# Performance work log

Measured on AMD Instinct MI355X. Metric: run time of the kernel, lower is better.

## Reference

```python
import jax, jax.numpy as jnp
import numpy as np

NUM_LAYERS = 2
MAG = 5 / 10.0  # magnitude=5 on a 0-10 scale
FILL = 0.5      # gray fill for out-of-bounds pixels (images in [0,1])
ENH = 1.0 + 0.9 * MAG  # enhancement factor magnitude (brightness/contrast/sharpness)


def _bilinear(img, xi, yi):
    H, W, _ = img.shape
    x0 = jnp.floor(xi); y0 = jnp.floor(yi)
    wx = xi - x0; wy = yi - y0
    def gather(yy, xx):
        valid = (xx >= 0) & (xx <= W - 1) & (yy >= 0) & (yy <= H - 1)
        v = img[jnp.clip(yy, 0, H - 1).astype(jnp.int32),
                jnp.clip(xx, 0, W - 1).astype(jnp.int32)]
        return jnp.where(valid[..., None], v, FILL)
    return (gather(y0, x0) * ((1 - wx) * (1 - wy))[..., None]
            + gather(y0, x0 + 1) * (wx * (1 - wy))[..., None]
            + gather(y0 + 1, x0) * ((1 - wx) * wy)[..., None]
            + gather(y0 + 1, x0 + 1) * (wx * wy)[..., None])


def _affine(img, a, b, tx, c, d, ty):
    # inverse affine map about image center, bilinear resample
    H, W, _ = img.shape
    ys, xs = jnp.meshgrid(jnp.arange(H, dtype=jnp.float32),
                          jnp.arange(W, dtype=jnp.float32), indexing='ij')
    cx = (W - 1) * 0.5; cy = (H - 1) * 0.5
    xi = a * (xs - cx) + b * (ys - cy) + tx + cx
    yi = c * (xs - cx) + d * (ys - cy) + ty + cy
    return _bilinear(img, xi, yi)


def _blend(a, b, f):
    return jnp.clip(a + f * (b - a), 0.0, 1.0)


def _smooth(img):
    # 3x3 smoothing kernel used by PIL/TF sharpness
    k = jnp.array([[1., 1., 1.], [1., 5., 1.], [1., 1., 1.]], jnp.float32) / 13.0
    H, W, _ = img.shape
    p = jnp.pad(img, ((1, 1), (1, 1), (0, 0)), mode='edge')
    out = jnp.zeros_like(img)
    for i in range(3):
        for j in range(3):
            out = out + k[i, j] * p[i:i + H, j:j + W]
    return out


def _rotate(img, s):
    th = s * (30.0 * MAG) * (np.pi / 180.0)
    co, si = jnp.cos(th), jnp.sin(th)
    return _affine(img, co, si, 0.0, -si, co, 0.0)

def _shear_x(img, s):
    sh = s * 0.3 * MAG
    return _affine(img, 1.0, -sh, 0.0, 0.0, 1.0, 0.0)

def _shear_y(img, s):
    sh = s * 0.3 * MAG
    return _affine(img, 1.0, 0.0, 0.0, -sh, 1.0, 0.0)

def _trans_x(img, s):
    t = s * 0.3 * MAG * img.shape[1]
    return _affine(img, 1.0, 0.0, -t, 0.0, 1.0, 0.0)

def _trans_y(img, s):
    t = s * 0.3 * MAG * img.shape[0]
    return _affine(img, 1.0, 0.0, 0.0, 0.0, 1.0, -t)

def _brightness(img, s):
    f = jnp.where(s > 0, ENH, 1.0 / ENH)
    return _blend(jnp.zeros_like(img), img, f)

def _contrast(img, s):
    f = jnp.where(s > 0, ENH, 1.0 / ENH)
    return _blend(jnp.mean(img) * jnp.ones_like(img), img, f)

def _sharpness(img, s):
    f = jnp.where(s > 0, ENH, 1.0 / ENH)
    return _blend(_smooth(img), img, f)


BRANCHES = [_rotate, _shear_x, _shear_y, _trans_x, _trans_y,
            _brightness, _contrast, _sharpness]


def _apply_one(img, ops, signs):
    # img: [H,W,3]; ops, signs: [NUM_LAYERS]
    for l in range(NUM_LAYERS):
        s = (2 * signs[l] - 1).astype(jnp.float32)
        img = jax.lax.switch(ops[l], BRANCHES, img, s)
    return img


def setup_inputs() -> dict:
    key = jax.random.key(0)
    k1, k2, k3 = jax.random.split(key, 3)
    B, H, W = 64, 512, 512
    images = jax.random.uniform(k1, (B, H, W, 3), dtype=jnp.float32)
    op_ids = jax.random.randint(k2, (B, NUM_LAYERS), 0, len(BRANCHES), dtype=jnp.int32)
    signs = jax.random.randint(k3, (B, NUM_LAYERS), 0, 2, dtype=jnp.int32)
    return {"images": images, "op_ids": op_ids, "signs": signs}


def reference(images, op_ids, signs):
    return jax.vmap(_apply_one)(images, op_ids, signs)
```

## Files before the change

### kernel.cpp

```cpp
#include <hip/hip_runtime.h>
#include <math.h>

#define IMH 512
#define IMW 512
#define NIMG 64
#define NPIX (IMH*IMW)
#define NELEM (NPIX*3)
#define CXF 255.5f
#define CYF 255.5f
#define ENHF 1.45f
#define INVENHF (1.0f/1.45f)
#define FILLF 0.5f
#define MBPI0 64
#define TW 32
#define TH 32
#define MAXLDS 1800

struct F3 { float x, y, z; };

__device__ __forceinline__ F3 mk3(float v){ F3 r; r.x=v; r.y=v; r.z=v; return r; }

__device__ __forceinline__ F3 ldpix(const float* __restrict__ im, int y, int x){
  const float* p = im + (y*IMW + x)*3;
  F3 r; r.x=p[0]; r.y=p[1]; r.z=p[2]; return r;
}

__device__ __forceinline__ F3 clip01(F3 v){
  F3 r;
  r.x = fminf(fmaxf(v.x, 0.f), 1.f);
  r.y = fminf(fmaxf(v.y, 0.f), 1.f);
  r.z = fminf(fmaxf(v.z, 0.f), 1.f);
  return r;
}

__device__ __forceinline__ void affine_params(int op, float s,
    float& a, float& b, float& tx, float& c, float& d, float& ty){
  a = 1.f; b = 0.f; tx = 0.f; c = 0.f; d = 1.f; ty = 0.f;
  if (op == 0){
    a = 0.96592582628907f; b = s * 0.25881904510252f; c = -b; d = a;
  } else if (op == 1){
    b = -s * 0.15f;
  } else if (op == 2){
    c = -s * 0.15f;
  } else if (op == 3){
    tx = -s * 76.8f;
  } else if (op == 4){
    ty = -s * 76.8f;
  }
}

__device__ __forceinline__ F3 bilin_img(const float* __restrict__ im, float xi, float yi){
  float x0f = floorf(xi), y0f = floorf(yi);
  float wx = xi - x0f, wy = yi - y0f;
  float w00 = (1.f-wx)*(1.f-wy), w01 = wx*(1.f-wy);
  float w10 = (1.f-wx)*wy,       w11 = wx*wy;
  int x0 = (int)x0f, y0 = (int)y0f;
  F3 r;
  if (x0 >= 0 && y0 >= 0 && x0 < IMW-1 && y0 < IMH-1){
    const float* p0 = im + (y0*IMW + x0)*3;
    const float* p1 = p0 + IMW*3;
    r.x = w00*p0[0] + w01*p0[3] + w10*p1[0] + w11*p1[3];
    r.y = w00*p0[1] + w01*p0[4] + w10*p1[1] + w11*p1[4];
    r.z = w00*p0[2] + w01*p0[5] + w10*p1[2] + w11*p1[5];
  } else {
    r = mk3(0.f);
    #pragma unroll
    for (int cidx = 0; cidx < 4; cidx++){
      int dx = cidx & 1, dy = cidx >> 1;
      int xx = x0 + dx, yy = y0 + dy;
      float w = (dx ? wx : (1.f - wx)) * (dy ? wy : (1.f - wy));
      F3 v;
      if (xx >= 0 && xx < IMW && yy >= 0 && yy < IMH)
        v = ldpix(im, yy, xx);
      else
        v = mk3(FILLF);
      r.x += w * v.x; r.y += w * v.y; r.z += w * v.z;
    }
  }
  return r;
}

__device__ F3 eval0(const float* __restrict__ im, int op, float s, float mean0, int x, int y){
  if (op < 5){
    float a,b,tx,c,d,ty; affine_params(op, s, a, b, tx, c, d, ty);
    float fx = (float)x - CXF, fy = (float)y - CYF;
    return bilin_img(im, a*fx + b*fy + tx + CXF, c*fx + d*fy + ty + CYF);
  }
  F3 v = ldpix(im, y, x);
  float f = (s > 0.f) ? ENHF : INVENHF;
  if (op == 5){
    F3 r; r.x = f*v.x; r.y = f*v.y; r.z = f*v.z; return clip01(r);
  }
  if (op == 6){
    F3 r;
    r.x = mean0 + f*(v.x - mean0);
    r.y = mean0 + f*(v.y - mean0);
    r.z = mean0 + f*(v.z - mean0);
    return clip01(r);
  }
  F3 sm; sm.x = (5.f/13.f)*v.x; sm.y = (5.f/13.f)*v.y; sm.z = (5.f/13.f)*v.z;
  #pragma unroll
  for (int dy = -1; dy <= 1; dy++){
    #pragma unroll
    for (int dx = -1; dx <= 1; dx++){
      if (dx == 0 && dy == 0) continue;
      int yy = min(max(y + dy, 0), IMH-1);
      int xx = min(max(x + dx, 0), IMW-1);
      F3 q = ldpix(im, yy, xx);
      sm.x += (1.f/13.f)*q.x; sm.y += (1.f/13.f)*q.y; sm.z += (1.f/13.f)*q.z;
    }
  }
  F3 r;
  r.x = sm.x + f*(v.x - sm.x);
  r.y = sm.y + f*(v.y - sm.y);
  r.z = sm.z + f*(v.z - sm.z);
  return clip01(r);
}

__device__ __forceinline__ float block_reduce(float v){
  #pragma unroll
  for (int off = 32; off > 0; off >>= 1) v += __shfl_down(v, off, 64);
  __shared__ float sm[4];
  int lane = threadIdx.x & 63, wid = threadIdx.x >> 6;
  if (lane == 0) sm[wid] = v;
  __syncthreads();
  float r = 0.f;
  if (threadIdx.x == 0) r = sm[0] + sm[1] + sm[2] + sm[3];
  return r;
}

__global__ __launch_bounds__(256) void mean0_kernel(const float* __restrict__ images,
    const int* __restrict__ ops, float* __restrict__ means){
  int img = blockIdx.x / MBPI0;
  if (ops[2*img] != 6) return;
  const float4* im = (const float4*)(images + (size_t)img * NELEM);
  float s = 0.f;
  for (int i = (blockIdx.x % MBPI0)*256 + threadIdx.x; i < NELEM/4; i += MBPI0*256){
    float4 v = im[i];
    s += v.x + v.y + v.z + v.w;
  }
  s = block_reduce(s);
  if (threadIdx.x == 0) atomicAdd(&means[2*img], s * (1.0f/(float)NELEM));
}

__device__ __forceinline__ void store4(float* __restrict__ out, int img, int y, int xbase,
                                       const F3* res){
  float4 o0 = make_float4(res[0].x, res[0].y, res[0].z, res[1].x);
  float4 o1 = make_float4(res[1].y, res[1].z, res[2].x, res[2].y);
  float4 o2 = make_float4(res[2].z, res[3].x, res[3].y, res[3].z);
  float4* op = (float4*)(out + ((size_t)img * NPIX + (size_t)y * IMW + xbase) * 3);
  op[0] = o0; op[1] = o1; op[2] = o2;
}

__global__ __launch_bounds__(256) void apply_kernel(const float* __restrict__ images,
    const int* __restrict__ ops, const int* __restrict__ signs,
    float* __restrict__ means, float* __restrict__ out){
  int img  = blockIdx.x >> 8;
  int tile = blockIdx.x & 255;
  int tx0 = (tile & 15) * TW;
  int ty0 = (tile >> 4) * TH;
  const float* im = images + (size_t)img * NELEM;
  int op0 = ops[2*img], op1 = ops[2*img + 1];
  float s0 = signs[2*img]     ? 1.f : -1.f;
  float s1 = signs[2*img + 1] ? 1.f : -1.f;
  float mean0 = means[2*img];

  int row   = threadIdx.x >> 3;
  int xbase = tx0 + ((threadIdx.x & 7) << 2);
  int y     = ty0 + row;
  float f1 = (s1 > 0.f) ? ENHF : INVENHF;

  if (op1 == 5 || op1 == 6){
    F3 res[4];
    float ssum = 0.f;
    #pragma unroll
    for (int q = 0; q < 4; q++){
      F3 v = eval0(im, op0, s0, mean0, xbase + q, y);
      if (op1 == 5){
        F3 o; o.x = f1*v.x; o.y = f1*v.y; o.z = f1*v.z;
        res[q] = clip01(o);
      } else {
        res[q] = v;
        ssum += v.x + v.y + v.z;
      }
    }
    store4(out, img, y, xbase, res);
    if (op1 == 6){
      ssum = block_reduce(ssum);
      if (threadIdx.x == 0) atomicAdd(&means[2*img + 1], ssum * (1.0f/(float)NELEM));
    }
    return;
  }

  float a1=1.f,b1=0.f,txx=0.f,c1=0.f,d1=1.f,tyy=0.f;
  int bx0, by0, bx1, by1;
  if (op1 < 5){
    affine_params(op1, s1, a1, b1, txx, c1, d1, tyy);
    float xmin = 1e30f, xmax = -1e30f, ymin = 1e30f, ymax = -1e30f;
    #pragma unroll
    for (int i = 0; i < 4; i++){
      float fx = (float)(tx0 + (i & 1) * (TW - 1)) - CXF;
      float fy = (float)(ty0 + (i >> 1) * (TH - 1)) - CYF;
      float xi = a1*fx + b1*fy + txx + CXF;
      float yi = c1*fx + d1*fy + tyy + CYF;
      xmin = fminf(xmin, xi); xmax = fmaxf(xmax, xi);
      ymin = fminf(ymin, yi); ymax = fmaxf(ymax, yi);
    }
    bx0 = (int)floorf(xmin) - 1; bx1 = (int)floorf(xmax) + 2;
    by0 = (int)floorf(ymin) - 1; by1 = (int)floorf(ymax) + 2;
  } else {
    bx0 = tx0 - 1; bx1 = tx0 + TW; by0 = ty0 - 1; by1 = ty0 + TH;
  }
  bx0 = max(bx0, 0); by0 = max(by0, 0);
  bx1 = min(bx1, IMW - 1); by1 = min(by1, IMH - 1);
  int bw = bx1 - bx0 + 1, bh = by1 - by0 + 1;
  int nstage = (bw > 0 && bh > 0) ? bw * bh : 0;

  __shared__ float lds[MAXLDS * 3];
  for (int idx = threadIdx.x; idx < nstage; idx += 256){
    int iy = idx / bw;
    int ix = idx - iy * bw;
    F3 v = eval0(im, op0, s0, mean0, bx0 + ix, by0 + iy);
    lds[idx*3 + 0] = v.x; lds[idx*3 + 1] = v.y; lds[idx*3 + 2] = v.z;
  }
  __syncthreads();

  F3 res[4];
  #pragma unroll
  for (int q = 0; q < 4; q++){
    int x = xbase + q;
    F3 o;
    if (op1 < 5){
      float fx = (float)x - CXF, fy = (float)y - CYF;
      float xi = a1*fx + b1*fy + txx + CXF;
      float yi = c1*fx + d1*fy + tyy + CYF;
      float xf0 = floorf(xi), yf0 = floorf(yi);
      float wx = xi - xf0, wy = yi - yf0;
      float w00 = (1.f-wx)*(1.f-wy), w01 = wx*(1.f-wy);
      float w10 = (1.f-wx)*wy,       w11 = wx*wy;
      int x0 = (int)xf0, y0 = (int)yf0;
      if (x0 >= 0 && y0 >= 0 && x0 < IMW-1 && y0 < IMH-1){
        const float* q0 = lds + ((y0 - by0) * bw + (x0 - bx0)) * 3;
        const float* q1 = q0 + bw * 3;
        o.x = w00*q0[0] + w01*q0[3] + w10*q1[0] + w11*q1[3];
        o.y = w00*q0[1] + w01*q0[4] + w10*q1[1] + w11*q1[4];
        o.z = w00*q0[2] + w01*q0[5] + w10*q1[2] + w11*q1[5];
      } else {
        o = mk3(0.f);
        #pragma unroll
        for (int ci = 0; ci < 4; ci++){
          int dx = ci & 1, dy = ci >> 1;
          int xx = x0 + dx, yy = y0 + dy;
          float w = (dx ? wx : (1.f - wx)) * (dy ? wy : (1.f - wy));
          F3 v;
          if (xx >= 0 && xx < IMW && yy >= 0 && yy < IMH){
            int li = ((yy - by0) * bw + (xx - bx0)) * 3;
            v.x = lds[li]; v.y = lds[li+1]; v.z = lds[li+2];
          } else v = mk3(FILLF);
          o.x += w * v.x; o.y += w * v.y; o.z += w * v.z;
        }
      }
    } else {
      int li0 = ((y - by0) * bw + (x - bx0)) * 3;
      F3 v; v.x = lds[li0]; v.y = lds[li0+1]; v.z = lds[li0+2];
      F3 sm; sm.x = (5.f/13.f)*v.x; sm.y = (5.f/13.f)*v.y; sm.z = (5.f/13.f)*v.z;
      #pragma unroll
      for (int dy = -1; dy <= 1; dy++){
        #pragma unroll
        for (int dx = -1; dx <= 1; dx++){
          if (dx == 0 && dy == 0) continue;
          int yy = min(max(y + dy, 0), IMH-1);
          int xx = min(max(x + dx, 0), IMW-1);
          int li = ((yy - by0) * bw + (xx - bx0)) * 3;
          sm.x += (1.f/13.f)*lds[li];
          sm.y += (1.f/13.f)*lds[li+1];
          sm.z += (1.f/13.f)*lds[li+2];
        }
      }
      o.x = sm.x + f1*(v.x - sm.x);
      o.y = sm.y + f1*(v.y - sm.y);
      o.z = sm.z + f1*(v.z - sm.z);
    }
    res[q] = clip01(o);
  }

  store4(out, img, y, xbase, res);
}

__global__ __launch_bounds__(256) void fixup_kernel(const int* __restrict__ ops,
    const int* __restrict__ signs, const float* __restrict__ means,
    float* __restrict__ out){
  int img = blockIdx.x >> 8;
  if (ops[2*img + 1] != 6) return;
  float f = signs[2*img + 1] ? ENHF : INVENHF;
  float m = means[2*img + 1];
  float4* p = (float4*)(out + (size_t)img * NELEM);
  const int n = NELEM / 4;
  for (int i = (blockIdx.x & 255)*256 + threadIdx.x; i < n; i += 256*256){
    float4 v = p[i];
    v.x = fminf(fmaxf(m + f*(v.x - m), 0.f), 1.f);
    v.y = fminf(fmaxf(m + f*(v.y - m), 0.f), 1.f);
    v.z = fminf(fmaxf(m + f*(v.z - m), 0.f), 1.f);
    v.w = fminf(fmaxf(m + f*(v.w - m), 0.f), 1.f);
    p[i] = v;
  }
}

extern "C" void kernel_launch(void* const* d_in, const int* in_sizes, int n_in,
                              void* d_out, int out_size, void* d_ws, size_t ws_size,
                              hipStream_t stream){
  const float* images = (const float*)d_in[0];
  const int*   ops    = (const int*)d_in[1];
  const int*   signs  = (const int*)d_in[2];
  float* out   = (float*)d_out;
  float* means = (float*)d_ws;

  hipMemsetAsync(means, 0, 2*NIMG*sizeof(float), stream);
  mean0_kernel<<<NIMG*MBPI0, 256, 0, stream>>>(images, ops, means);
  apply_kernel<<<NIMG*256, 256, 0, stream>>>(images, ops, signs, means, out);
  fixup_kernel<<<NIMG*256, 256, 0, stream>>>(ops, signs, means, out);
}
```

Before: 409.4 us.

## Add tile-level interior fast paths and tighter LDS staging for layer-two resample

```diff
diff --git a/kernel.cpp b/kernel.cpp
--- a/kernel.cpp
+++ b/kernel.cpp
@@ -14,7 +14,7 @@
 #define MBPI0 64
 #define TW 32
 #define TH 32
-#define MAXLDS 1800
+#define MAXLDS 1700
 
 struct F3 { float x, y, z; };
 
@@ -49,33 +49,39 @@
   }
 }
 
+__device__ __forceinline__ F3 bilin_interior(const float* __restrict__ im, float xi, float yi){
+  float x0f = floorf(xi), y0f = floorf(yi);
+  float wx = xi - x0f, wy = yi - y0f;
+  float w00=(1.f-wx)*(1.f-wy), w01=wx*(1.f-wy), w10=(1.f-wx)*wy, w11=wx*wy;
+  const float* p0 = im + ((int)y0f*IMW + (int)x0f)*3;
+  const float* p1 = p0 + IMW*3;
+  F3 r;
+  r.x = w00*p0[0]+w01*p0[3]+w10*p1[0]+w11*p1[3];
+  r.y = w00*p0[1]+w01*p0[4]+w10*p1[1]+w11*p1[4];
+  r.z = w00*p0[2]+w01*p0[5]+w10*p1[2]+w11*p1[5];
+  return r;
+}
+
 __device__ __forceinline__ F3 bilin_img(const float* __restrict__ im, float xi, float yi){
   float x0f = floorf(xi), y0f = floorf(yi);
   float wx = xi - x0f, wy = yi - y0f;
-  float w00 = (1.f-wx)*(1.f-wy), w01 = wx*(1.f-wy);
-  float w10 = (1.f-wx)*wy,       w11 = wx*wy;
   int x0 = (int)x0f, y0 = (int)y0f;
   F3 r;
   if (x0 >= 0 && y0 >= 0 && x0 < IMW-1 && y0 < IMH-1){
-    const float* p0 = im + (y0*IMW + x0)*3;
-    const float* p1 = p0 + IMW*3;
-    r.x = w00*p0[0] + w01*p0[3] + w10*p1[0] + w11*p1[3];
-    r.y = w00*p0[1] + w01*p0[4] + w10*p1[1] + w11*p1[4];
-    r.z = w00*p0[2] + w01*p0[5] + w10*p1[2] + w11*p1[5];
-  } else {
-    r = mk3(0.f);
-    #pragma unroll
-    for (int cidx = 0; cidx < 4; cidx++){
-      int dx = cidx & 1, dy = cidx >> 1;
-      int xx = x0 + dx, yy = y0 + dy;
-      float w = (dx ? wx : (1.f - wx)) * (dy ? wy : (1.f - wy));
-      F3 v;
-      if (xx >= 0 && xx < IMW && yy >= 0 && yy < IMH)
-        v = ldpix(im, yy, xx);
-      else
-        v = mk3(FILLF);
-      r.x += w * v.x; r.y += w * v.y; r.z += w * v.z;
-    }
+    return bilin_interior(im, xi, yi);
+  }
+  r = mk3(0.f);
+  #pragma unroll
+  for (int cidx = 0; cidx < 4; cidx++){
+    int dx = cidx & 1, dy = cidx >> 1;
+    int xx = x0 + dx, yy = y0 + dy;
+    float w = (dx ? wx : (1.f - wx)) * (dy ? wy : (1.f - wy));
+    F3 v;
+    if (xx >= 0 && xx < IMW && yy >= 0 && yy < IMH)
+      v = ldpix(im, yy, xx);
+    else
+      v = mk3(FILLF);
+    r.x += w * v.x; r.y += w * v.y; r.z += w * v.z;
   }
   return r;
 }
@@ -152,7 +158,7 @@
   op[0] = o0; op[1] = o1; op[2] = o2;
 }
 
-__global__ __launch_bounds__(256) void apply_kernel(const float* __restrict__ images,
+__global__ __launch_bounds__(256, 8) void apply_kernel(const float* __restrict__ images,
     const int* __restrict__ ops, const int* __restrict__ signs,
     float* __restrict__ means, float* __restrict__ out){
   int img  = blockIdx.x >> 8;
@@ -171,17 +177,48 @@
   float f1 = (s1 > 0.f) ? ENHF : INVENHF;
 
   if (op1 == 5 || op1 == 6){
+    F3 v4[4];
+    if (op0 < 5){
+      float a0,b0,t0x,c0,d0,t0y; affine_params(op0, s0, a0,b0,t0x,c0,d0,t0y);
+      float fxl = (float)tx0 - CXF, fxr = (float)(tx0+TW-1) - CXF;
+      float fyt = (float)ty0 - CYF, fyb = (float)(ty0+TH-1) - CYF;
+      float xA = a0*fxl + b0*fyt, xB = a0*fxr + b0*fyt, xC = a0*fxl + b0*fyb, xD = a0*fxr + b0*fyb;
+      float yA = c0*fxl + d0*fyt, yB = c0*fxr + d0*fyt, yC = c0*fxl + d0*fyb, yD = c0*fxr + d0*fyb;
+      float sxmin = fminf(fminf(xA,xB),fminf(xC,xD)) + t0x + CXF;
+      float sxmax = fmaxf(fmaxf(xA,xB),fmaxf(xC,xD)) + t0x + CXF;
+      float symin = fminf(fminf(yA,yB),fminf(yC,yD)) + t0y + CYF;
+      float symax = fmaxf(fmaxf(yA,yB),fmaxf(yC,yD)) + t0y + CYF;
+      bool inter = (sxmin >= 1.f) && (symin >= 1.f) &&
+                   (sxmax <= (float)(IMW-2)) && (symax <= (float)(IMH-2));
+      float fy = (float)y - CYF;
+      if (inter){
+        #pragma unroll
+        for (int q = 0; q < 4; q++){
+          float fx = (float)(xbase + q) - CXF;
+          v4[q] = bilin_interior(im, a0*fx + b0*fy + t0x + CXF, c0*fx + d0*fy + t0y + CYF);
+        }
+      } else {
+        #pragma unroll
+        for (int q = 0; q < 4; q++){
+          float fx = (float)(xbase + q) - CXF;
+          v4[q] = bilin_img(im, a0*fx + b0*fy + t0x + CXF, c0*fx + d0*fy + t0y + CYF);
+        }
+      }
+    } else {
+      #pragma unroll
+      for (int q = 0; q < 4; q++)
+        v4[q] = eval0(im, op0, s0, mean0, xbase + q, y);
+    }
     F3 res[4];
     float ssum = 0.f;
     #pragma unroll
     for (int q = 0; q < 4; q++){
-      F3 v = eval0(im, op0, s0, mean0, xbase + q, y);
       if (op1 == 5){
-        F3 o; o.x = f1*v.x; o.y = f1*v.y; o.z = f1*v.z;
+        F3 o; o.x = f1*v4[q].x; o.y = f1*v4[q].y; o.z = f1*v4[q].z;
         res[q] = clip01(o);
       } else {
-        res[q] = v;
-        ssum += v.x + v.y + v.z;
+        res[q] = v4[q];
+        ssum += v4[q].x + v4[q].y + v4[q].z;
       }
     }
     store4(out, img, y, xbase, res);
@@ -193,7 +230,7 @@
   }
 
   float a1=1.f,b1=0.f,txx=0.f,c1=0.f,d1=1.f,tyy=0.f;
-  int bx0, by0, bx1, by1;
+  int pbx0, pby0, pbx1, pby1;
   if (op1 < 5){
     affine_params(op1, s1, a1, b1, txx, c1, d1, tyy);
     float xmin = 1e30f, xmax = -1e30f, ymin = 1e30f, ymax = -1e30f;
@@ -206,82 +243,132 @@
       xmin = fminf(xmin, xi); xmax = fmaxf(xmax, xi);
       ymin = fminf(ymin, yi); ymax = fmaxf(ymax, yi);
     }
-    bx0 = (int)floorf(xmin) - 1; bx1 = (int)floorf(xmax) + 2;
-    by0 = (int)floorf(ymin) - 1; by1 = (int)floorf(ymax) + 2;
+    pbx0 = (int)floorf(xmin); pbx1 = (int)floorf(xmax) + 1;
+    pby0 = (int)floorf(ymin); pby1 = (int)floorf(ymax) + 1;
   } else {
-    bx0 = tx0 - 1; bx1 = tx0 + TW; by0 = ty0 - 1; by1 = ty0 + TH;
-  }
-  bx0 = max(bx0, 0); by0 = max(by0, 0);
-  bx1 = min(bx1, IMW - 1); by1 = min(by1, IMH - 1);
+    pbx0 = tx0 - 1; pbx1 = tx0 + TW; pby0 = ty0 - 1; pby1 = ty0 + TH;
+  }
+  int bx0 = max(pbx0, 0), by0 = max(pby0, 0);
+  int bx1 = min(pbx1, IMW - 1), by1 = min(pby1, IMH - 1);
   int bw = bx1 - bx0 + 1, bh = by1 - by0 + 1;
   int nstage = (bw > 0 && bh > 0) ? bw * bh : 0;
+  bool l1_interior = (op1 < 5) && pbx0 >= 0 && pby0 >= 0 && pbx1 <= IMW-1 && pby1 <= IMH-1;
 
   __shared__ float lds[MAXLDS * 3];
-  for (int idx = threadIdx.x; idx < nstage; idx += 256){
-    int iy = idx / bw;
-    int ix = idx - iy * bw;
-    F3 v = eval0(im, op0, s0, mean0, bx0 + ix, by0 + iy);
-    lds[idx*3 + 0] = v.x; lds[idx*3 + 1] = v.y; lds[idx*3 + 2] = v.z;
+  if (nstage > 0){
+    int Kq = 256 / bw, Rr = 256 - Kq * bw;
+    int iy = (int)threadIdx.x / bw;
+    int ix = (int)threadIdx.x - iy * bw;
+    if (op0 < 5){
+      float a0,b0,t0x,c0,d0,t0y; affine_params(op0, s0, a0,b0,t0x,c0,d0,t0y);
+      float Cx = a0*((float)bx0 - CXF) + b0*((float)by0 - CYF) + t0x + CXF;
+      float Cy = c0*((float)bx0 - CXF) + d0*((float)by0 - CYF) + t0y + CYF;
+      float w = (float)(bw - 1), h = (float)(bh - 1);
+      float x00 = Cx, x10 = Cx + a0*w, x01 = Cx + b0*h, x11 = Cx + a0*w + b0*h;
+      float y00 = Cy, y10 = Cy + c0*w, y01 = Cy + d0*h, y11 = Cy + c0*w + d0*h;
+      float sxmin = fminf(fminf(x00,x10),fminf(x01,x11));
+      float sxmax = fmaxf(fmaxf(x00,x10),fmaxf(x01,x11));
+      float symin = fminf(fminf(y00,y10),fminf(y01,y11));
+      float symax = fmaxf(fmaxf(y00,y10),fmaxf(y01,y11));
+      bool inter = (sxmin >= 1.f) && (symin >= 1.f) &&
+                   (sxmax <= (float)(IMW-2)) && (symax <= (float)(IMH-2));
+      if (inter){
+        for (int idx = threadIdx.x; idx < nstage; idx += 256){
+          float xi = a0*(float)ix + b0*(float)iy + Cx;
+          float yi = c0*(float)ix + d0*(float)iy + Cy;
+          F3 v = bilin_interior(im, xi, yi);
+          lds[idx*3+0]=v.x; lds[idx*3+1]=v.y; lds[idx*3+2]=v.z;
+          ix += Rr; iy += Kq; if (ix >= bw){ ix -= bw; iy += 1; }
+        }
+      } else {
+        for (int idx = threadIdx.x; idx < nstage; idx += 256){
+          float xi = a0*(float)ix + b0*(float)iy + Cx;
+          float yi = c0*(float)ix + d0*(float)iy + Cy;
+          F3 v = bilin_img(im, xi, yi);
+          lds[idx*3+0]=v.x; lds[idx*3+1]=v.y; lds[idx*3+2]=v.z;
+          ix += Rr; iy += Kq; if (ix >= bw){ ix -= bw; iy += 1; }
+        }
+      }
+    } else {
+      for (int idx = threadIdx.x; idx < nstage; idx += 256){
+        F3 v = eval0(im, op0, s0, mean0, bx0 + ix, by0 + iy);
+        lds[idx*3+0]=v.x; lds[idx*3+1]=v.y; lds[idx*3+2]=v.z;
+        ix += Rr; iy += Kq; if (ix >= bw){ ix -= bw; iy += 1; }
+      }
+    }
   }
   __syncthreads();
 
   F3 res[4];
-  #pragma unroll
-  for (int q = 0; q < 4; q++){
-    int x = xbase + q;
-    F3 o;
-    if (op1 < 5){
-      float fx = (float)x - CXF, fy = (float)y - CYF;
+  if (op1 < 5 && l1_interior){
+    float fy = (float)y - CYF;
+    #pragma unroll
+    for (int q = 0; q < 4; q++){
+      float fx = (float)(xbase + q) - CXF;
       float xi = a1*fx + b1*fy + txx + CXF;
       float yi = c1*fx + d1*fy + tyy + CYF;
-      float xf0 = floorf(xi), yf0 = floorf(yi);
-      float wx = xi - xf0, wy = yi - yf0;
-      float w00 = (1.f-wx)*(1.f-wy), w01 = wx*(1.f-wy);
-      float w10 = (1.f-wx)*wy,       w11 = wx*wy;
-      int x0 = (int)xf0, y0 = (int)yf0;
-      if (x0 >= 0 && y0 >= 0 && x0 < IMW-1 && y0 < IMH-1){
-        const float* q0 = lds + ((y0 - by0) * bw + (x0 - bx0)) * 3;
-        const float* q1 = q0 + bw * 3;
-        o.x = w00*q0[0] + w01*q0[3] + w10*q1[0] + w11*q1[3];
-        o.y = w00*q0[1] + w01*q0[4] + w10*q1[1] + w11*q1[4];
-        o.z = w00*q0[2] + w01*q0[5] + w10*q1[2] + w11*q1[5];
-      } else {
+      float x0f = fminf(fmaxf(floorf(xi), (float)bx0), (float)(bx1-1));
+      float y0f = fminf(fmaxf(floorf(yi), (float)by0), (float)(by1-1));
+      float wx = xi - x0f, wy = yi - y0f;
+      float w00=(1.f-wx)*(1.f-wy), w01=wx*(1.f-wy), w10=(1.f-wx)*wy, w11=wx*wy;
+      const float* q0 = lds + (((int)y0f - by0) * bw + ((int)x0f - bx0)) * 3;
+      const float* q1 = q0 + bw * 3;
+      F3 o;
+      o.x = w00*q0[0] + w01*q0[3] + w10*q1[0] + w11*q1[3];
+      o.y = w00*q0[1] + w01*q0[4] + w10*q1[1] + w11*q1[4];
+      o.z = w00*q0[2] + w01*q0[5] + w10*q1[2] + w11*q1[5];
+      res[q] = clip01(o);
+    }
+  } else {
+    #pragma unroll
+    for (int q = 0; q < 4; q++){
+      int x = xbase + q;
+      F3 o;
+      if (op1 < 5){
+        float fx = (float)x - CXF, fy = (float)y - CYF;
+        float xi = a1*fx + b1*fy + txx + CXF;
+        float yi = c1*fx + d1*fy + tyy + CYF;
+        float xf0 = floorf(xi), yf0 = floorf(yi);
+        float wx = xi - xf0, wy = yi - yf0;
+        int x0 = (int)xf0, y0 = (int)yf0;
         o = mk3(0.f);
         #pragma unroll
         for (int ci = 0; ci < 4; ci++){
           int dx = ci & 1, dy = ci >> 1;
           int xx = x0 + dx, yy = y0 + dy;
-          float w = (dx ? wx : (1.f - wx)) * (dy ? wy : (1.f - wy));
+          float wq = (dx ? wx : (1.f - wx)) * (dy ? wy : (1.f - wy));
           F3 v;
           if (xx >= 0 && xx < IMW && yy >= 0 && yy < IMH){
-            int li = ((yy - by0) * bw + (xx - bx0)) * 3;
+            int lx = min(max(xx - bx0, 0), bw - 1);
+            int ly = min(max(yy - by0, 0), bh - 1);
+            int li = (ly * bw + lx) * 3;
             v.x = lds[li]; v.y = lds[li+1]; v.z = lds[li+2];
           } else v = mk3(FILLF);
-          o.x += w * v.x; o.y += w * v.y; o.z += w * v.z;
-        }
+          o.x += wq * v.x; o.y += wq * v.y; o.z += wq * v.z;
+        }
+      } else {
+        int li0 = ((y - by0) * bw + (x - bx0)) * 3;
+        F3 v; v.x = lds[li0]; v.y = lds[li0+1]; v.z = lds[li0+2];
+        F3 sm; sm.x = (5.f/13.f)*v.x; sm.y = (5.f/13.f)*v.y; sm.z = (5.f/13.f)*v.z;
+        #pragma unroll
+        for (int dy = -1; dy <= 1; dy++){
+          #pragma unroll
+          for (int dx = -1; dx <= 1; dx++){
+            if (dx == 0 && dy == 0) continue;
+            int yy = min(max(y + dy, 0), IMH-1);
+            int xx = min(max(x + dx, 0), IMW-1);
+            int li = ((yy - by0) * bw + (xx - bx0)) * 3;
+            sm.x += (1.f/13.f)*lds[li];
+            sm.y += (1.f/13.f)*lds[li+1];
+            sm.z += (1.f/13.f)*lds[li+2];
+          }
+        }
+        o.x = sm.x + f1*(v.x - sm.x);
+        o.y = sm.y + f1*(v.y - sm.y);
+        o.z = sm.z + f1*(v.z - sm.z);
       }
-    } else {
-      int li0 = ((y - by0) * bw + (x - bx0)) * 3;
-      F3 v; v.x = lds[li0]; v.y = lds[li0+1]; v.z = lds[li0+2];
-      F3 sm; sm.x = (5.f/13.f)*v.x; sm.y = (5.f/13.f)*v.y; sm.z = (5.f/13.f)*v.z;
-      #pragma unroll
-      for (int dy = -1; dy <= 1; dy++){
-        #pragma unroll
-        for (int dx = -1; dx <= 1; dx++){
-          if (dx == 0 && dy == 0) continue;
-          int yy = min(max(y + dy, 0), IMH-1);
-          int xx = min(max(x + dx, 0), IMW-1);
-          int li = ((yy - by0) * bw + (xx - bx0)) * 3;
-          sm.x += (1.f/13.f)*lds[li];
-          sm.y += (1.f/13.f)*lds[li+1];
-          sm.z += (1.f/13.f)*lds[li+2];
-        }
-      }
-      o.x = sm.x + f1*(v.x - sm.x);
-      o.y = sm.y + f1*(v.y - sm.y);
-      o.z = sm.z + f1*(v.z - sm.z);
-    }
-    res[q] = clip01(o);
+      res[q] = clip01(o);
+    }
   }
 
   store4(out, img, y, xbase, res);
```

Measured after the change: 401.2 us. -2.0%, faster.
